# Performance work log

Measured on AMD Instinct MI355X. Metric: run time of the kernel, lower is better.

The kernel has to match this reference:

```python
import jax, jax.numpy as jnp
import numpy as np

B, T, V, H, E, F, NM = 128, 32, 10000, 512, 512, 2048, 512
D0 = E + NM + H   # 1536: layer-0 concat(x, h)
D1 = H + H        # 1024: layer-1 concat(h_prev_layer, h)


def setup_inputs() -> dict:
    key = jax.random.key(0)
    ks = jax.random.split(key, 10)
    cnn_features = jax.random.normal(ks[0], (B, F), jnp.float32)
    x_tokens = jax.random.randint(ks[1], (B, T), 0, V)
    current_hidden_state = jnp.zeros((2, B, 2 * H), jnp.float32)
    embedding = jax.random.normal(ks[2], (V, E), jnp.float32)
    W_in = jax.random.normal(ks[3], (F, NM), jnp.float32) / np.sqrt(F)
    b_in = jnp.zeros((NM,), jnp.float32)
    # 4 gates stacked (order: i, o, f, c) -- same math as 4 separate matmuls
    W0 = jax.random.normal(ks[4], (D0, 4 * H), jnp.float32) / np.sqrt(D0)
    b0 = jnp.full((4 * H,), 2.0, jnp.float32)
    W1 = jax.random.normal(ks[5], (D1, 4 * H), jnp.float32) / np.sqrt(D1)
    b1 = jnp.full((4 * H,), 2.0, jnp.float32)
    W_out = jax.random.normal(ks[6], (H, V), jnp.float32) / np.sqrt(H)
    b_out = jnp.zeros((V,), jnp.float32)
    return {"cnn_features": cnn_features, "x_tokens": x_tokens,
            "current_hidden_state": current_hidden_state, "embedding": embedding,
            "W_in": W_in, "b_in": b_in, "W0": W0, "b0": b0,
            "W1": W1, "b1": b1, "W_out": W_out, "b_out": b_out,
            "is_train": 1}


def _lstm_gates(z, c_prev):
    # gate order i, o, f, c matches the original cell's separate matmuls
    i_t, o_t, f_t, c_hat = jnp.split(z, 4, axis=1)
    i_t = jax.nn.sigmoid(i_t)
    o_t = jax.nn.sigmoid(o_t)
    f_t = jax.nn.sigmoid(f_t)
    c_hat = jnp.tanh(c_hat)
    c_t = f_t * c_prev + i_t * c_hat
    h_t = o_t * jnp.tanh(c_t)
    return h_t, c_t


def reference(cnn_features, x_tokens, current_hidden_state, embedding,
              W_in, b_in, W0, b0, W1, b1, W_out, b_out, is_train):
    # input_layer: Dropout (identity in eval) -> Linear -> LeakyReLU(0.01)
    proc = jax.nn.leaky_relu(cnn_features @ W_in + b_in, negative_slope=0.01)  # [B, NM]
    emb = embedding[x_tokens]  # [B, T, E] (teacher forcing: is_train=True)

    def step(hidden, emb_t):
        # layer 0: input = concat(token_emb, processed cnn features)
        x0 = jnp.concatenate([emb_t, proc], axis=1)          # [B, E+NM]
        h0, c0 = hidden[0, :, :H], hidden[0, :, H:]
        z0 = jnp.concatenate([x0, h0], axis=1) @ W0 + b0     # [B, 4H]
        h0n, c0n = _lstm_gates(z0, c0)
        # layer 1: input = h of layer 0 (already updated this timestep)
        h1, c1 = hidden[1, :, :H], hidden[1, :, H:]
        z1 = jnp.concatenate([h0n, h1], axis=1) @ W1 + b1    # [B, 4H]
        h1n, c1n = _lstm_gates(z1, c1)
        logits_t = h1n @ W_out + b_out                        # [B, V]
        new_hidden = jnp.stack([jnp.concatenate([h0n, c0n], axis=1),
                                jnp.concatenate([h1n, c1n], axis=1)], axis=0)
        return new_hidden, logits_t

    hidden, logits_seq = jax.lax.scan(step, current_hidden_state,
                                      jnp.moveaxis(emb, 1, 0))  # scan over T
    logits = jnp.moveaxis(logits_seq, 0, 1)  # [B, T, V]
    return logits, hidden
```

## Files before the change

kernel.cpp:

```cpp
#include <hip/hip_runtime.h>


typedef short s8v __attribute__((ext_vector_type(8)));
typedef float f4v __attribute__((ext_vector_type(4)));

__device__ __forceinline__ unsigned short f2bf(float f) {
  unsigned u = __float_as_uint(f);
  u += 0x7fffu + ((u >> 16) & 1u);
  return (unsigned short)(u >> 16);
}
__device__ __forceinline__ float sigm(float x) { return 1.0f / (1.0f + __expf(-x)); }
__device__ __forceinline__ float tanh_(float x) { return 1.0f - 2.0f / (1.0f + __expf(2.0f * x)); }

__device__ __forceinline__ void glds16(const unsigned short* g, unsigned short* l) {
  __builtin_amdgcn_global_load_lds((const __attribute__((address_space(1))) void*)g,
                                   (__attribute__((address_space(3))) void*)l, 16, 0, 0);
}

__global__ void k_transpose_cvt(const float* __restrict__ src, unsigned short* __restrict__ dst,
                                int R, int C) {
  __shared__ float tile[32][33];
  int c0 = blockIdx.x * 32, r0 = blockIdx.y * 32;
  int tx = threadIdx.x, ty = threadIdx.y;
#pragma unroll
  for (int i = 0; i < 4; i++) {
    int r = r0 + ty + i * 8, c = c0 + tx;
    if (r < R && c < C) tile[ty + i * 8][tx] = src[(size_t)r * C + c];
  }
  __syncthreads();
#pragma unroll
  for (int i = 0; i < 4; i++) {
    int c = c0 + ty + i * 8, r = r0 + tx;
    if (r < R && c < C) dst[(size_t)c * R + r] = f2bf(tile[tx][ty + i * 8]);
  }
}

__global__ void k_cvt_bf16(const float* __restrict__ in, unsigned short* __restrict__ out, int n4) {
  int i = blockIdx.x * 256 + threadIdx.x;
  if (i >= n4) return;
  float4 v = ((const float4*)in)[i];
  ushort4 p; p.x = f2bf(v.x); p.y = f2bf(v.y); p.z = f2bf(v.z); p.w = f2bf(v.w);
  ((ushort4*)out)[i] = p;
}

__global__ void k_gather_emb(const float* __restrict__ emb, const int* __restrict__ tok,
                             unsigned short* __restrict__ Xe) {
  int i = blockIdx.x * 256 + threadIdx.x;
  int r = i >> 7, k4 = (i & 127) * 4;
  int b = r & 127, t = r >> 7;
  int tk = tok[b * 32 + t];
  float4 v = *(const float4*)(emb + (size_t)tk * 512 + k4);
  ushort4 p; p.x = f2bf(v.x); p.y = f2bf(v.y); p.z = f2bf(v.z); p.w = f2bf(v.w);
  ((ushort4*)Xe)[i] = p;
}

__global__ void k_init_state(const float* __restrict__ chs,
                             unsigned short* __restrict__ h0b1, unsigned short* __restrict__ h1b1,
                             float* __restrict__ h0f, float* __restrict__ c0f,
                             float* __restrict__ h1f, float* __restrict__ c1f) {
  int i = blockIdx.x * 256 + threadIdx.x;
  int b = i >> 9, j = i & 511;
  float h0 = chs[b * 1024 + j], c0 = chs[b * 1024 + 512 + j];
  float h1 = chs[131072 + b * 1024 + j], c1 = chs[131072 + b * 1024 + 512 + j];
  h0f[i] = h0; c0f[i] = c0; h1f[i] = h1; c1f[i] = c1;
  h0b1[i] = f2bf(h0); h1b1[i] = f2bf(h1);
}

template <int MODE>
__global__ __launch_bounds__(256, 2)
void k_gemm(const unsigned short* __restrict__ A, const unsigned short* __restrict__ Bt,
            const float* __restrict__ bias, const float* __restrict__ add128,
            float* __restrict__ outF, unsigned short* __restrict__ outB,
            int M, int N, int K) {
  __shared__ unsigned short As[4096];
  __shared__ unsigned short Bs[4096];
  int tid = threadIdx.x;
  int wave = tid >> 6, lane = tid & 63;
  int lr = lane & 15, lq = lane >> 4;
  int wm = (wave >> 1) * 64, wn = (wave & 1) * 64;
  int m0 = blockIdx.y * 128, n0 = blockIdx.x * 128;

  f4v acc[4][4];
  f4v zero = {0.0f, 0.0f, 0.0f, 0.0f};
#pragma unroll
  for (int i = 0; i < 4; i++)
#pragma unroll
    for (int j = 0; j < 4; j++) acc[i][j] = zero;

  int srow = tid >> 2, sofs = (tid & 3) * 8;
  int ar0 = m0 + srow, ar1 = ar0 + 64;
  int br0 = n0 + srow, br1 = br0 + 64;
  if (br0 >= N) br0 = N - 1;
  if (br1 >= N) br1 = N - 1;
  const unsigned short* Ag0 = A + (size_t)ar0 * K + sofs;
  const unsigned short* Ag1 = A + (size_t)ar1 * K + sofs;
  const unsigned short* Bg0 = Bt + (size_t)br0 * K + sofs;
  const unsigned short* Bg1 = Bt + (size_t)br1 * K + sofs;
  unsigned short* lA0 = &As[tid * 8];
  unsigned short* lA1 = &As[2048 + tid * 8];
  unsigned short* lB0 = &Bs[tid * 8];
  unsigned short* lB1 = &Bs[2048 + tid * 8];

  for (int k0 = 0; k0 < K; k0 += 32) {
    glds16(Ag0 + k0, lA0);
    glds16(Ag1 + k0, lA1);
    glds16(Bg0 + k0, lB0);
    glds16(Bg1 + k0, lB1);
    __syncthreads();
    s8v af[4], bfr[4];
#pragma unroll
    for (int i = 0; i < 4; i++) af[i] = *(const s8v*)&As[(wm + i * 16 + lr) * 32 + lq * 8];
#pragma unroll
    for (int i = 0; i < 4; i++) bfr[i] = *(const s8v*)&Bs[(wn + i * 16 + lr) * 32 + lq * 8];
#pragma unroll
    for (int i = 0; i < 4; i++)
#pragma unroll
      for (int j = 0; j < 4; j++)
        acc[i][j] = __builtin_amdgcn_mfma_f32_16x16x32_bf16(af[i], bfr[j], acc[i][j], 0, 0, 0);
    __syncthreads();
  }

#pragma unroll
  for (int i = 0; i < 4; i++) {
#pragma unroll
    for (int j = 0; j < 4; j++) {
      int nn = n0 + wn + j * 16 + lr;
      if (nn >= N) continue;
#pragma unroll
      for (int r = 0; r < 4; r++) {
        int mm = m0 + wm + i * 16 + lq * 4 + r;
        float v = acc[i][j][r];
        if (MODE == 0) {
          v += bias[nn];
          v = v > 0.0f ? v : 0.01f * v;
          outB[(size_t)mm * N + nn] = f2bf(v);
        } else if (MODE == 1) {
          v += bias[nn];
          outF[(size_t)mm * N + nn] = v;
        } else if (MODE == 2) {
          v += add128[(size_t)(mm & 127) * N + nn];
          outF[(size_t)mm * N + nn] = v;
        } else {
          v += bias[nn];
          int b = mm & 127, t = mm >> 7;
          outF[(size_t)(b * 32 + t) * N + nn] = v;
        }
      }
    }
  }
}

__global__ __launch_bounds__(128)
void k_phase(const unsigned short* __restrict__ W0h_t, const unsigned short* __restrict__ W1_t,
             const float* __restrict__ Zx, const float* __restrict__ b1,
             unsigned short* __restrict__ h0b0, unsigned short* __restrict__ h0b1,
             unsigned short* __restrict__ h1b0, unsigned short* __restrict__ h1b1,
             float* __restrict__ h0f, float* __restrict__ c0f,
             float* __restrict__ h1f, float* __restrict__ c1f,
             unsigned short* __restrict__ H1all,
             int tB, int doB, int tA, int doA) {
  int wave = threadIdx.x >> 6, lane = threadIdx.x & 63;
  int gid = blockIdx.x * 2 + wave;
  bool isB = gid < 256;
  if (isB && !doB) return;
  if (!isB && !doA) return;
  int id = gid & 255;
  int mt = id >> 5, jt = id & 31;
  int lr = lane & 15, lq = lane >> 4;
  int m = mt * 16 + lr;
  f4v zero = {0.0f, 0.0f, 0.0f, 0.0f};
  f4v acc[4] = {zero, zero, zero, zero};

  if (isB) {
    const unsigned short* h0r = (tB & 1) ? h0b1 : h0b0;
    const unsigned short* h1r = (tB & 1) ? h1b0 : h1b1;
    unsigned short* h1w = (tB & 1) ? h1b1 : h1b0;
    for (int kc = 0; kc < 32; kc++) {
      int kk = kc * 32 + lq * 8;
      const unsigned short* ap = (kk < 512) ? (h0r + m * 512 + kk)
                                            : (h1r + m * 512 + kk - 512);
      s8v a = *(const s8v*)ap;
#pragma unroll
      for (int g = 0; g < 4; g++) {
        int n = g * 512 + jt * 16 + lr;
        s8v b = *(const s8v*)(W1_t + (size_t)n * 1024 + kc * 32 + lq * 8);
        acc[g] = __builtin_amdgcn_mfma_f32_16x16x32_bf16(a, b, acc[g], 0, 0, 0);
      }
    }
    int j = jt * 16 + lr;
    float bi = b1[j], bo = b1[512 + j], bff = b1[1024 + j], bc = b1[1536 + j];
#pragma unroll
    for (int r = 0; r < 4; r++) {
      int mm = mt * 16 + lq * 4 + r;
      int idx = mm * 512 + j;
      float cprev = c1f[idx];
      float iv = sigm(acc[0][r] + bi);
      float ov = sigm(acc[1][r] + bo);
      float fv = sigm(acc[2][r] + bff);
      float cv = tanh_(acc[3][r] + bc);
      float cn = fv * cprev + iv * cv;
      float hn = ov * tanh_(cn);
      c1f[idx] = cn; h1f[idx] = hn;
      unsigned short hb = f2bf(hn);
      h1w[idx] = hb;
      H1all[(size_t)(tB * 128 + mm) * 512 + j] = hb;
    }
  } else {
    const unsigned short* h0r = (tA & 1) ? h0b0 : h0b1;
    unsigned short* h0w = (tA & 1) ? h0b1 : h0b0;
    for (int kc = 0; kc < 16; kc++) {
      s8v a = *(const s8v*)(h0r + m * 512 + kc * 32 + lq * 8);
#pragma unroll
      for (int g = 0; g < 4; g++) {
        int n = g * 512 + jt * 16 + lr;
        s8v b = *(const s8v*)(W0h_t + (size_t)n * 512 + kc * 32 + lq * 8);
        acc[g] = __builtin_amdgcn_mfma_f32_16x16x32_bf16(a, b, acc[g], 0, 0, 0);
      }
    }
    int j = jt * 16 + lr;
    const float* zrow = Zx + (size_t)tA * 128 * 2048;
#pragma unroll
    for (int r = 0; r < 4; r++) {
      int mm = mt * 16 + lq * 4 + r;
      int idx = mm * 512 + j;
      float cprev = c0f[idx];
      float iv = sigm(acc[0][r] + zrow[mm * 2048 + j]);
      float ov = sigm(acc[1][r] + zrow[mm * 2048 + 512 + j]);
      float fv = sigm(acc[2][r] + zrow[mm * 2048 + 1024 + j]);
      float cv = tanh_(acc[3][r] + zrow[mm * 2048 + 1536 + j]);
      float cn = fv * cprev + iv * cv;
      float hn = ov * tanh_(cn);
      c0f[idx] = cn; h0f[idx] = hn;
      h0w[idx] = f2bf(hn);
    }
  }
}

__global__ void k_write_hidden(const float* __restrict__ h0f, const float* __restrict__ c0f,
                               const float* __restrict__ h1f, const float* __restrict__ c1f,
                               float* __restrict__ out) {
  int idx = blockIdx.x * 256 + threadIdx.x;
  int l = idx >> 17, rem = idx & 131071, b = rem >> 10, j = rem & 1023;
  const float* hs = l ? h1f : h0f;
  const float* cs = l ? c1f : c0f;
  float v = (j < 512) ? hs[b * 512 + j] : cs[b * 512 + (j - 512)];
  out[40960000 + idx] = v;
}

extern "C" void kernel_launch(void* const* d_in, const int* in_sizes, int n_in,
                              void* d_out, int out_size, void* d_ws, size_t ws_size,
                              hipStream_t stream) {
  const float* cnn  = (const float*)d_in[0];
  const int*   tok  = (const int*)d_in[1];
  const float* chs  = (const float*)d_in[2];
  const float* emb  = (const float*)d_in[3];
  const float* W_in = (const float*)d_in[4];
  const float* b_in = (const float*)d_in[5];
  const float* W0   = (const float*)d_in[6];
  const float* b0   = (const float*)d_in[7];
  const float* W1   = (const float*)d_in[8];
  const float* b1   = (const float*)d_in[9];
  const float* W_out= (const float*)d_in[10];
  const float* b_out= (const float*)d_in[11];
  float* out = (float*)d_out;

  char* p = (char*)d_ws;
  auto alloc = [&](size_t bytes) { char* q = p; p += (bytes + 255) & ~(size_t)255; return q; };
  unsigned short* Win_t  = (unsigned short*)alloc((size_t)512 * 2048 * 2);
  unsigned short* W0e_t  = (unsigned short*)alloc((size_t)2048 * 512 * 2);
  unsigned short* W0m_t  = (unsigned short*)alloc((size_t)2048 * 512 * 2);
  unsigned short* W0h_t  = (unsigned short*)alloc((size_t)2048 * 512 * 2);
  unsigned short* W1_t   = (unsigned short*)alloc((size_t)2048 * 1024 * 2);
  unsigned short* Wout_t = (unsigned short*)alloc((size_t)10000 * 512 * 2);
  unsigned short* cnn_b  = (unsigned short*)alloc((size_t)128 * 2048 * 2);
  unsigned short* proc_b = (unsigned short*)alloc((size_t)128 * 512 * 2);
  float*          Cf     = (float*)alloc((size_t)128 * 2048 * 4);
  unsigned short* Xe     = (unsigned short*)alloc((size_t)4096 * 512 * 2);
  float*          Zx     = (float*)alloc((size_t)4096 * 2048 * 4);
  unsigned short* h0b0   = (unsigned short*)alloc(65536 * 2);
  unsigned short* h0b1   = (unsigned short*)alloc(65536 * 2);
  unsigned short* h1b0   = (unsigned short*)alloc(65536 * 2);
  unsigned short* h1b1   = (unsigned short*)alloc(65536 * 2);
  float*          h0f    = (float*)alloc(65536 * 4);
  float*          c0f    = (float*)alloc(65536 * 4);
  float*          h1f    = (float*)alloc(65536 * 4);
  float*          c1f    = (float*)alloc(65536 * 4);
  unsigned short* H1all  = (unsigned short*)alloc((size_t)4096 * 512 * 2);

  dim3 tb(32, 8);
  k_transpose_cvt<<<dim3(16, 64),  tb, 0, stream>>>(W_in, Win_t, 2048, 512);
  k_transpose_cvt<<<dim3(64, 16),  tb, 0, stream>>>(W0,               W0e_t, 512, 2048);
  k_transpose_cvt<<<dim3(64, 16),  tb, 0, stream>>>(W0 + 512 * 2048,  W0m_t, 512, 2048);
  k_transpose_cvt<<<dim3(64, 16),  tb, 0, stream>>>(W0 + 1024 * 2048, W0h_t, 512, 2048);
  k_transpose_cvt<<<dim3(64, 32),  tb, 0, stream>>>(W1, W1_t, 1024, 2048);
  k_transpose_cvt<<<dim3(313, 16), tb, 0, stream>>>(W_out, Wout_t, 512, 10000);
  k_cvt_bf16<<<256, 256, 0, stream>>>(cnn, cnn_b, 65536);

  k_gemm<0><<<dim3(4, 1), 256, 0, stream>>>(cnn_b, Win_t, b_in, nullptr, nullptr, proc_b,
                                            128, 512, 2048);
  k_gemm<1><<<dim3(16, 1), 256, 0, stream>>>(proc_b, W0m_t, b0, nullptr, Cf, nullptr,
                                             128, 2048, 512);
  k_gather_emb<<<2048, 256, 0, stream>>>(emb, tok, Xe);
  k_gemm<2><<<dim3(16, 32), 256, 0, stream>>>(Xe, W0e_t, nullptr, Cf, Zx, nullptr,
                                              4096, 2048, 512);
  k_init_state<<<256, 256, 0, stream>>>(chs, h0b1, h1b1, h0f, c0f, h1f, c1f);

  k_phase<<<256, 128, 0, stream>>>(W0h_t, W1_t, Zx, b1, h0b0, h0b1, h1b0, h1b1,
                                   h0f, c0f, h1f, c1f, H1all, 0, 0, 0, 1);
  for (int t = 0; t < 32; t++)
    k_phase<<<256, 128, 0, stream>>>(W0h_t, W1_t, Zx, b1, h0b0, h0b1, h1b0, h1b1,
                                     h0f, c0f, h1f, c1f, H1all, t, 1, t + 1, (t < 31) ? 1 : 0);

  k_gemm<3><<<dim3(79, 32), 256, 0, stream>>>(H1all, Wout_t, b_out, nullptr, out, nullptr,
                                              4096, 10000, 512);
  k_write_hidden<<<1024, 256, 0, stream>>>(h0f, c0f, h1f, c1f, out);
}
```

Measured before the change: 872.6 us.

## Replace per-step LSTM launches with persistent kernel using grid barrier

The 33 per-timestep phase kernel launches are replaced by one persistent kernel of 256 blocks that loops over time and synchronises through a flag-based grid barrier in global memory. K is split across the four waves with an LDS reduction, and cell state is kept in registers instead of global float buffers. Final hidden and cell values are written straight to the output, so the separate write-hidden kernel goes away. This removes launch overhead and state round-trips, but relies on all 256 blocks being co-resident and adds spin-barrier cost at every step.

```diff
diff --git a/kernel.cpp b/kernel.cpp
--- a/kernel.cpp
+++ b/kernel.cpp
@@ -3,6 +3,8 @@
 
 typedef short s8v __attribute__((ext_vector_type(8)));
 typedef float f4v __attribute__((ext_vector_type(4)));
+
+#define OUT_H 40960000
 
 __device__ __forceinline__ unsigned short f2bf(float f) {
   unsigned u = __float_as_uint(f);
@@ -54,16 +56,14 @@
   ((ushort4*)Xe)[i] = p;
 }
 
-__global__ void k_init_state(const float* __restrict__ chs,
-                             unsigned short* __restrict__ h0b1, unsigned short* __restrict__ h1b1,
-                             float* __restrict__ h0f, float* __restrict__ c0f,
-                             float* __restrict__ h1f, float* __restrict__ c1f) {
+__global__ void k_init2(const float* __restrict__ chs,
+                        unsigned short* __restrict__ h0b1, unsigned short* __restrict__ h1b1,
+                        int* __restrict__ bar) {
   int i = blockIdx.x * 256 + threadIdx.x;
   int b = i >> 9, j = i & 511;
-  float h0 = chs[b * 1024 + j], c0 = chs[b * 1024 + 512 + j];
-  float h1 = chs[131072 + b * 1024 + j], c1 = chs[131072 + b * 1024 + 512 + j];
-  h0f[i] = h0; c0f[i] = c0; h1f[i] = h1; c1f[i] = c1;
-  h0b1[i] = f2bf(h0); h1b1[i] = f2bf(h1);
+  h0b1[i] = f2bf(chs[b * 1024 + j]);
+  h1b1[i] = f2bf(chs[131072 + b * 1024 + j]);
+  if (i < 4096) bar[i] = 0;
 }
 
 template <int MODE>
@@ -150,101 +150,150 @@
   }
 }
 
-__global__ __launch_bounds__(128)
-void k_phase(const unsigned short* __restrict__ W0h_t, const unsigned short* __restrict__ W1_t,
-             const float* __restrict__ Zx, const float* __restrict__ b1,
-             unsigned short* __restrict__ h0b0, unsigned short* __restrict__ h0b1,
-             unsigned short* __restrict__ h1b0, unsigned short* __restrict__ h1b1,
-             float* __restrict__ h0f, float* __restrict__ c0f,
-             float* __restrict__ h1f, float* __restrict__ c1f,
-             unsigned short* __restrict__ H1all,
-             int tB, int doB, int tA, int doA) {
-  int wave = threadIdx.x >> 6, lane = threadIdx.x & 63;
-  int gid = blockIdx.x * 2 + wave;
-  bool isB = gid < 256;
-  if (isB && !doB) return;
-  if (!isB && !doA) return;
-  int id = gid & 255;
-  int mt = id >> 5, jt = id & 31;
+template <int NKC>
+__device__ __forceinline__ void pmm(const unsigned short* __restrict__ hA,
+                                    const unsigned short* __restrict__ w0,
+                                    const unsigned short* __restrict__ w1,
+                                    const unsigned short* __restrict__ w2,
+                                    const unsigned short* __restrict__ w3,
+                                    int am0, int am1, int ko, f4v acc[2][4]) {
+#pragma unroll
+  for (int kc = 0; kc < NKC; kc++) {
+    int kk = kc * 32 + ko;
+    s8v a0 = *(const s8v*)(hA + am0 * 512 + kk);
+    s8v a1 = *(const s8v*)(hA + am1 * 512 + kk);
+    s8v b0 = *(const s8v*)(w0 + kk);
+    s8v b1 = *(const s8v*)(w1 + kk);
+    s8v b2 = *(const s8v*)(w2 + kk);
+    s8v b3 = *(const s8v*)(w3 + kk);
+    acc[0][0] = __builtin_amdgcn_mfma_f32_16x16x32_bf16(a0, b0, acc[0][0], 0, 0, 0);
+    acc[1][0] = __builtin_amdgcn_mfma_f32_16x16x32_bf16(a1, b0, acc[1][0], 0, 0, 0);
+    acc[0][1] = __builtin_amdgcn_mfma_f32_16x16x32_bf16(a0, b1, acc[0][1], 0, 0, 0);
+    acc[1][1] = __builtin_amdgcn_mfma_f32_16x16x32_bf16(a1, b1, acc[1][1], 0, 0, 0);
+    acc[0][2] = __builtin_amdgcn_mfma_f32_16x16x32_bf16(a0, b2, acc[0][2], 0, 0, 0);
+    acc[1][2] = __builtin_amdgcn_mfma_f32_16x16x32_bf16(a1, b2, acc[1][2], 0, 0, 0);
+    acc[0][3] = __builtin_amdgcn_mfma_f32_16x16x32_bf16(a0, b3, acc[0][3], 0, 0, 0);
+    acc[1][3] = __builtin_amdgcn_mfma_f32_16x16x32_bf16(a1, b3, acc[1][3], 0, 0, 0);
+  }
+}
+
+__device__ __forceinline__ void gridbar(int* bar, int gen) {
+  __syncthreads();
+  if (threadIdx.x == 0) {
+    __threadfence();
+    __hip_atomic_store(&bar[blockIdx.x * 16], gen, __ATOMIC_RELAXED, __HIP_MEMORY_SCOPE_AGENT);
+  }
+  while (__hip_atomic_load(&bar[threadIdx.x * 16], __ATOMIC_RELAXED, __HIP_MEMORY_SCOPE_AGENT) < gen) {}
+  __syncthreads();
+  if (threadIdx.x == 0) __threadfence();
+  __syncthreads();
+}
+
+__global__ __launch_bounds__(256, 2)
+void k_lstm(const unsigned short* __restrict__ W0h_t, const unsigned short* __restrict__ W1_t,
+            const float* __restrict__ Zx, const float* __restrict__ b1,
+            const float* __restrict__ chs,
+            unsigned short* __restrict__ h0b0, unsigned short* __restrict__ h0b1,
+            unsigned short* __restrict__ h1b0, unsigned short* __restrict__ h1b1,
+            unsigned short* __restrict__ H1all, float* __restrict__ outHid,
+            int* __restrict__ bar) {
+  __shared__ f4v part[8][4][64];
+  int tid = threadIdx.x;
+  int wave = tid >> 6, lane = tid & 63;
   int lr = lane & 15, lq = lane >> 4;
-  int m = mt * 16 + lr;
-  f4v zero = {0.0f, 0.0f, 0.0f, 0.0f};
-  f4v acc[4] = {zero, zero, zero, zero};
-
-  if (isB) {
-    const unsigned short* h0r = (tB & 1) ? h0b1 : h0b0;
-    const unsigned short* h1r = (tB & 1) ? h1b0 : h1b1;
-    unsigned short* h1w = (tB & 1) ? h1b1 : h1b0;
-    for (int kc = 0; kc < 32; kc++) {
-      int kk = kc * 32 + lq * 8;
-      const unsigned short* ap = (kk < 512) ? (h0r + m * 512 + kk)
-                                            : (h1r + m * 512 + kk - 512);
-      s8v a = *(const s8v*)ap;
+  int bb = blockIdx.x;
+  bool isB = bb < 128;
+  int gb = isB ? bb : bb - 128;
+  int jt = gb >> 2, mh = gb & 3;
+  int kq = wave;
+  int j = jt * 16 + lr;
+  int Kfull = isB ? 1024 : 512;
+  int kbase = kq * (Kfull >> 2);
+  int am0 = (mh * 2) * 16 + lr;
+  int am1 = (mh * 2 + 1) * 16 + lr;
+  int me_base = (mh * 2 + wave) * 16 + lq * 4;
+
+  const unsigned short* Wt = isB ? W1_t : W0h_t;
+  const unsigned short* wg0 = Wt + (size_t)(0 * 512 + jt * 16 + lr) * Kfull + kbase;
+  const unsigned short* wg1 = Wt + (size_t)(1 * 512 + jt * 16 + lr) * Kfull + kbase;
+  const unsigned short* wg2 = Wt + (size_t)(2 * 512 + jt * 16 + lr) * Kfull + kbase;
+  const unsigned short* wg3 = Wt + (size_t)(3 * 512 + jt * 16 + lr) * Kfull + kbase;
+
+  float cs[4] = {0, 0, 0, 0};
+  float bi = 0, bo = 0, bf_ = 0, bc = 0;
+  if (wave < 2) {
+    int coff = isB ? 131072 : 0;
+#pragma unroll
+    for (int r = 0; r < 4; r++) cs[r] = chs[coff + (size_t)(me_base + r) * 1024 + 512 + j];
+    if (isB) { bi = b1[j]; bo = b1[512 + j]; bf_ = b1[1024 + j]; bc = b1[1536 + j]; }
+  }
+
+  for (int p = 0; p <= 32; p++) {
+    int t = isB ? (p - 1) : p;
+    bool active = isB ? (p >= 1) : (p <= 31);
+    f4v acc[2][4];
+    if (active) {
+      const unsigned short* hA;
+      if (isB) {
+        const unsigned short* h0r = (t & 1) ? h0b1 : h0b0;
+        const unsigned short* h1r = (t & 1) ? h1b0 : h1b1;
+        hA = (kbase < 512) ? (h0r + kbase) : (h1r + kbase - 512);
+      } else {
+        hA = ((t & 1) ? h0b0 : h0b1) + kbase;
+      }
+      f4v zero = {0.0f, 0.0f, 0.0f, 0.0f};
+#pragma unroll
+      for (int i = 0; i < 2; i++)
+#pragma unroll
+        for (int g = 0; g < 4; g++) acc[i][g] = zero;
+      if (isB) pmm<8>(hA, wg0, wg1, wg2, wg3, am0, am1, lq * 8, acc);
+      else     pmm<4>(hA, wg0, wg1, wg2, wg3, am0, am1, lq * 8, acc);
+#pragma unroll
+      for (int i = 0; i < 2; i++)
+#pragma unroll
+        for (int g = 0; g < 4; g++) part[kq * 2 + i][g][lane] = acc[i][g];
+    }
+    __syncthreads();
+    if (active && wave < 2) {
+      f4v z[4];
 #pragma unroll
       for (int g = 0; g < 4; g++) {
-        int n = g * 512 + jt * 16 + lr;
-        s8v b = *(const s8v*)(W1_t + (size_t)n * 1024 + kc * 32 + lq * 8);
-        acc[g] = __builtin_amdgcn_mfma_f32_16x16x32_bf16(a, b, acc[g], 0, 0, 0);
+        f4v s = part[wave][g][lane];
+        s += part[2 + wave][g][lane];
+        s += part[4 + wave][g][lane];
+        s += part[6 + wave][g][lane];
+        z[g] = s;
+      }
+      unsigned short* hw;
+      if (isB) hw = (t & 1) ? h1b1 : h1b0;
+      else     hw = (t & 1) ? h0b1 : h0b0;
+#pragma unroll
+      for (int r = 0; r < 4; r++) {
+        int m = me_base + r;
+        float zi, zo, zf, zc;
+        if (isB) {
+          zi = z[0][r] + bi; zo = z[1][r] + bo; zf = z[2][r] + bf_; zc = z[3][r] + bc;
+        } else {
+          const float* zrow = Zx + (size_t)t * 262144 + (size_t)m * 2048;
+          zi = z[0][r] + zrow[j];        zo = z[1][r] + zrow[512 + j];
+          zf = z[2][r] + zrow[1024 + j]; zc = z[3][r] + zrow[1536 + j];
+        }
+        float iv = sigm(zi), ov = sigm(zo), fv = sigm(zf), cv = tanh_(zc);
+        float cn = fv * cs[r] + iv * cv;
+        float hn = ov * tanh_(cn);
+        cs[r] = cn;
+        unsigned short hb = f2bf(hn);
+        hw[m * 512 + j] = hb;
+        if (isB) H1all[((size_t)t * 128 + m) * 512 + j] = hb;
+        if (t == 31) {
+          size_t o = OUT_H + (isB ? 131072 : 0) + (size_t)m * 1024;
+          outHid[o + j] = hn;
+          outHid[o + 512 + j] = cn;
+        }
       }
     }
-    int j = jt * 16 + lr;
-    float bi = b1[j], bo = b1[512 + j], bff = b1[1024 + j], bc = b1[1536 + j];
-#pragma unroll
-    for (int r = 0; r < 4; r++) {
-      int mm = mt * 16 + lq * 4 + r;
-      int idx = mm * 512 + j;
-      float cprev = c1f[idx];
-      float iv = sigm(acc[0][r] + bi);
-      float ov = sigm(acc[1][r] + bo);
-      float fv = sigm(acc[2][r] + bff);
-      float cv = tanh_(acc[3][r] + bc);
-      float cn = fv * cprev + iv * cv;
-      float hn = ov * tanh_(cn);
-      c1f[idx] = cn; h1f[idx] = hn;
-      unsigned short hb = f2bf(hn);
-      h1w[idx] = hb;
-      H1all[(size_t)(tB * 128 + mm) * 512 + j] = hb;
-    }
-  } else {
-    const unsigned short* h0r = (tA & 1) ? h0b0 : h0b1;
-    unsigned short* h0w = (tA & 1) ? h0b1 : h0b0;
-    for (int kc = 0; kc < 16; kc++) {
-      s8v a = *(const s8v*)(h0r + m * 512 + kc * 32 + lq * 8);
-#pragma unroll
-      for (int g = 0; g < 4; g++) {
-        int n = g * 512 + jt * 16 + lr;
-        s8v b = *(const s8v*)(W0h_t + (size_t)n * 512 + kc * 32 + lq * 8);
-        acc[g] = __builtin_amdgcn_mfma_f32_16x16x32_bf16(a, b, acc[g], 0, 0, 0);
-      }
-    }
-    int j = jt * 16 + lr;
-    const float* zrow = Zx + (size_t)tA * 128 * 2048;
-#pragma unroll
-    for (int r = 0; r < 4; r++) {
-      int mm = mt * 16 + lq * 4 + r;
-      int idx = mm * 512 + j;
-      float cprev = c0f[idx];
-      float iv = sigm(acc[0][r] + zrow[mm * 2048 + j]);
-      float ov = sigm(acc[1][r] + zrow[mm * 2048 + 512 + j]);
-      float fv = sigm(acc[2][r] + zrow[mm * 2048 + 1024 + j]);
-      float cv = tanh_(acc[3][r] + zrow[mm * 2048 + 1536 + j]);
-      float cn = fv * cprev + iv * cv;
-      float hn = ov * tanh_(cn);
-      c0f[idx] = cn; h0f[idx] = hn;
-      h0w[idx] = f2bf(hn);
-    }
-  }
-}
-
-__global__ void k_write_hidden(const float* __restrict__ h0f, const float* __restrict__ c0f,
-                               const float* __restrict__ h1f, const float* __restrict__ c1f,
-                               float* __restrict__ out) {
-  int idx = blockIdx.x * 256 + threadIdx.x;
-  int l = idx >> 17, rem = idx & 131071, b = rem >> 10, j = rem & 1023;
-  const float* hs = l ? h1f : h0f;
-  const float* cs = l ? c1f : c0f;
-  float v = (j < 512) ? hs[b * 512 + j] : cs[b * 512 + (j - 512)];
-  out[40960000 + idx] = v;
+    if (p < 32) gridbar(bar, p + 1);
+  }
 }
 
 extern "C" void kernel_launch(void* const* d_in, const int* in_sizes, int n_in,
@@ -281,11 +330,8 @@
   unsigned short* h0b1   = (unsigned short*)alloc(65536 * 2);
   unsigned short* h1b0   = (unsigned short*)alloc(65536 * 2);
   unsigned short* h1b1   = (unsigned short*)alloc(65536 * 2);
-  float*          h0f    = (float*)alloc(65536 * 4);
-  float*          c0f    = (float*)alloc(65536 * 4);
-  float*          h1f    = (float*)alloc(65536 * 4);
-  float*          c1f    = (float*)alloc(65536 * 4);
   unsigned short* H1all  = (unsigned short*)alloc((size_t)4096 * 512 * 2);
+  int*            bar    = (int*)alloc(4096 * 4);
 
   dim3 tb(32, 8);
   k_transpose_cvt<<<dim3(16, 64),  tb, 0, stream>>>(W_in, Win_t, 2048, 512);
@@ -303,15 +349,11 @@
   k_gather_emb<<<2048, 256, 0, stream>>>(emb, tok, Xe);
   k_gemm<2><<<dim3(16, 32), 256, 0, stream>>>(Xe, W0e_t, nullptr, Cf, Zx, nullptr,
                                               4096, 2048, 512);
-  k_init_state<<<256, 256, 0, stream>>>(chs, h0b1, h1b1, h0f, c0f, h1f, c1f);
-
-  k_phase<<<256, 128, 0, stream>>>(W0h_t, W1_t, Zx, b1, h0b0, h0b1, h1b0, h1b1,
-                                   h0f, c0f, h1f, c1f, H1all, 0, 0, 0, 1);
-  for (int t = 0; t < 32; t++)
-    k_phase<<<256, 128, 0, stream>>>(W0h_t, W1_t, Zx, b1, h0b0, h0b1, h1b0, h1b1,
-                                     h0f, c0f, h1f, c1f, H1all, t, 1, t + 1, (t < 31) ? 1 : 0);
+  k_init2<<<256, 256, 0, stream>>>(chs, h0b1, h1b1, bar);
+
+  k_lstm<<<256, 256, 0, stream>>>(W0h_t, W1_t, Zx, b1, chs,
+                                  h0b0, h0b1, h1b0, h1b1, H1all, out, bar);
 
   k_gemm<3><<<dim3(79, 32), 256, 0, stream>>>(H1all, Wout_t, b_out, nullptr, out, nullptr,
                                               4096, 10000, 512);
-  k_write_hidden<<<1024, 256, 0, stream>>>(h0f, c0f, h1f, c1f, out);
-}
+}
```

After: 992.6 us. +13.7%, slower.
